# Performance work log

Measured on AMD Instinct MI355X. Metric: run time of the kernel, lower is better.

The kernel has to match this reference:

```python
import jax, jax.numpy as jnp
import numpy as np

# per-position segment id for seq_len=16: slices [0:1],[1:6],[6:9],[9:10],[10:16]
SEG = np.array([0] + [1]*5 + [2]*3 + [3] + [4]*6, dtype=np.int32)
HEAD_DIM = 3
NUM_HEADS = 2


def setup_inputs() -> dict:
    key = jax.random.key(0)
    ks = jax.random.split(key, 9)
    B = 262144
    s = 1.0 / np.sqrt(6.0)  # torch Linear init scale
    return {
        "x": jax.random.normal(ks[0], (B, 16, 6), dtype=jnp.float32),
        "Wq": jax.random.uniform(ks[1], (5, 6, 6), jnp.float32, -s, s),
        "bq": jax.random.uniform(ks[2], (5, 6), jnp.float32, -s, s),
        "Wk": jax.random.uniform(ks[3], (5, 6, 6), jnp.float32, -s, s),
        "bk": jax.random.uniform(ks[4], (5, 6), jnp.float32, -s, s),
        "Wv": jax.random.uniform(ks[5], (5, 6, 6), jnp.float32, -s, s),
        "bv": jax.random.uniform(ks[6], (5, 6), jnp.float32, -s, s),
        "Wo": jax.random.uniform(ks[7], (6, 6), jnp.float32, -s, s),
        "bo": jax.random.uniform(ks[8], (6,), jnp.float32, -s, s),
    }


def reference(x, Wq, bq, Wk, bk, Wv, bv, Wo, bo):
    B, S, D = x.shape  # S=16, D=6
    seg = jnp.asarray(SEG)

    def seg_proj(W, b):
        # torch Linear: y = x @ W.T + b; gather per-position segment weights
        return jnp.einsum('bsd,sod->bso', x, W[seg]) + b[seg]

    def heads(t):
        return t.reshape(B, S, NUM_HEADS, HEAD_DIM).transpose(0, 2, 1, 3)

    Q = heads(seg_proj(Wq, bq))  # [B,H,S,hd]
    K = heads(seg_proj(Wk, bk))
    V = heads(seg_proj(Wv, bv))

    scores = jnp.einsum('bhqd,bhkd->bhqk', Q, K) / jnp.sqrt(jnp.float32(HEAD_DIM))
    attn = jax.nn.softmax(scores, axis=-1)
    ctx = jnp.einsum('bhqk,bhkd->bhqd', attn, V)
    ctx = ctx.transpose(0, 2, 1, 3).reshape(B, S, D)
    return ctx @ Wo.T + bo
```

## Files before the change

### kernel.cpp

```cpp
#include <hip/hip_runtime.h>

#define SCALE 0.57735026918962576f

#define OFF_WQ 0
#define OFF_BQ 260
#define OFF_WK 300
#define OFF_BK 560
#define OFF_WV 600
#define OFF_BV 860
#define OFF_WO 900
#define OFF_BO 948
#define OFF_K  956
#define OFF_V  3068
#define GSTRIDE 132
#define LDS_FLOATS 5180

__global__ __launch_bounds__(256) void attn_seg_kernel(
    const float* __restrict__ x,
    const float* __restrict__ Wq, const float* __restrict__ bq,
    const float* __restrict__ Wk, const float* __restrict__ bk,
    const float* __restrict__ Wv, const float* __restrict__ bv,
    const float* __restrict__ Wo, const float* __restrict__ bo,
    float* __restrict__ out, int total)
{
    __shared__ __align__(16) float lds[LDS_FLOATS];
    const int t = threadIdx.x;

    if (t < 180) {
        unsigned sg = (unsigned)t / 36u, r = (unsigned)t - sg * 36u;
        unsigned o = r / 6u, d = r - o * 6u;
        int dst = (int)(sg * 52u + o * 8u + d);
        lds[OFF_WQ + dst] = Wq[t];
        lds[OFF_WK + dst] = Wk[t];
        lds[OFF_WV + dst] = Wv[t];
    }
    if (t < 30) {
        unsigned sg = (unsigned)t / 6u, o = (unsigned)t - sg * 6u;
        lds[OFF_BQ + sg * 8u + o] = bq[t];
        lds[OFF_BK + sg * 8u + o] = bk[t];
        lds[OFF_BV + sg * 8u + o] = bv[t];
    }
    if (t < 36) {
        unsigned o = (unsigned)t / 6u, d = (unsigned)t - o * 6u;
        lds[OFF_WO + o * 8u + d] = Wo[t];
    }
    if (t < 6) lds[OFF_BO + t] = bo[t];

    const int g = t >> 4;
    const int s = t & 15;
    const int seg = (s == 0) ? 0 : (s < 6) ? 1 : (s < 9) ? 2 : (s == 9) ? 3 : 4;

    const int pos = blockIdx.x * 256 + t;
    const bool valid = pos < total;
    float x0=0.f,x1=0.f,x2=0.f,x3=0.f,x4=0.f,x5=0.f;
    if (valid) {
        const float* xp = x + (size_t)pos * 6;
        float2 a = *(const float2*)(xp);
        float2 b = *(const float2*)(xp + 2);
        float2 c = *(const float2*)(xp + 4);
        x0=a.x; x1=a.y; x2=b.x; x3=b.y; x4=c.x; x5=c.y;
    }

    __syncthreads();

    float q[6], kk[6], vv[6];
    {
        const float* W = &lds[OFF_WQ + seg * 52];
        float4 b4 = *(const float4*)&lds[OFF_BQ + seg * 8];
        float2 b2 = *(const float2*)&lds[OFF_BQ + seg * 8 + 4];
        float bb[6] = {b4.x, b4.y, b4.z, b4.w, b2.x, b2.y};
        #pragma unroll
        for (int o = 0; o < 6; o++) {
            float4 w4 = *(const float4*)(W + o * 8);
            float2 w2 = *(const float2*)(W + o * 8 + 4);
            q[o] = bb[o] + x0*w4.x + x1*w4.y + x2*w4.z + x3*w4.w + x4*w2.x + x5*w2.y;
        }
    }
    {
        const float* W = &lds[OFF_WK + seg * 52];
        float4 b4 = *(const float4*)&lds[OFF_BK + seg * 8];
        float2 b2 = *(const float2*)&lds[OFF_BK + seg * 8 + 4];
        float bb[6] = {b4.x, b4.y, b4.z, b4.w, b2.x, b2.y};
        #pragma unroll
        for (int o = 0; o < 6; o++) {
            float4 w4 = *(const float4*)(W + o * 8);
            float2 w2 = *(const float2*)(W + o * 8 + 4);
            kk[o] = bb[o] + x0*w4.x + x1*w4.y + x2*w4.z + x3*w4.w + x4*w2.x + x5*w2.y;
        }
    }
    {
        const float* W = &lds[OFF_WV + seg * 52];
        float4 b4 = *(const float4*)&lds[OFF_BV + seg * 8];
        float2 b2 = *(const float2*)&lds[OFF_BV + seg * 8 + 4];
        float bb[6] = {b4.x, b4.y, b4.z, b4.w, b2.x, b2.y};
        #pragma unroll
        for (int o = 0; o < 6; o++) {
            float4 w4 = *(const float4*)(W + o * 8);
            float2 w2 = *(const float2*)(W + o * 8 + 4);
            vv[o] = bb[o] + x0*w4.x + x1*w4.y + x2*w4.z + x3*w4.w + x4*w2.x + x5*w2.y;
        }
    }

    {
        float* Kd = &lds[OFF_K + g * GSTRIDE + s * 8];
        *(float4*)Kd       = make_float4(kk[0], kk[1], kk[2], kk[3]);
        *(float2*)(Kd + 4) = make_float2(kk[4], kk[5]);
        float* Vd = &lds[OFF_V + g * GSTRIDE + s * 8];
        *(float4*)Vd       = make_float4(vv[0], vv[1], vv[2], vv[3]);
        *(float2*)(Vd + 4) = make_float2(vv[4], vv[5]);
    }

    __syncthreads();

    #pragma unroll
    for (int i = 0; i < 6; i++) q[i] *= SCALE;

    float sc0[16], sc1[16];
    {
        const float* Kb = &lds[OFF_K + g * GSTRIDE];
        #pragma unroll
        for (int k = 0; k < 16; k++) {
            float4 a = *(const float4*)(Kb + k * 8);
            float2 b = *(const float2*)(Kb + k * 8 + 4);
            sc0[k] = q[0]*a.x + q[1]*a.y + q[2]*a.z;
            sc1[k] = q[3]*a.w + q[4]*b.x + q[5]*b.y;
        }
    }

    float m0 = sc0[0], m1 = sc1[0];
    #pragma unroll
    for (int k = 1; k < 16; k++) { m0 = fmaxf(m0, sc0[k]); m1 = fmaxf(m1, sc1[k]); }
    float sum0 = 0.f, sum1 = 0.f;
    #pragma unroll
    for (int k = 0; k < 16; k++) {
        float e0 = __expf(sc0[k] - m0); sc0[k] = e0; sum0 += e0;
        float e1 = __expf(sc1[k] - m1); sc1[k] = e1; sum1 += e1;
    }
    const float inv0 = __builtin_amdgcn_rcpf(sum0);
    const float inv1 = __builtin_amdgcn_rcpf(sum1);

    float c0=0.f,c1=0.f,c2=0.f,c3=0.f,c4=0.f,c5=0.f;
    {
        const float* Vb = &lds[OFF_V + g * GSTRIDE];
        #pragma unroll
        for (int k = 0; k < 16; k++) {
            float4 a = *(const float4*)(Vb + k * 8);
            float2 b = *(const float2*)(Vb + k * 8 + 4);
            c0 += sc0[k]*a.x; c1 += sc0[k]*a.y; c2 += sc0[k]*a.z;
            c3 += sc1[k]*a.w; c4 += sc1[k]*b.x; c5 += sc1[k]*b.y;
        }
    }
    c0 *= inv0; c1 *= inv0; c2 *= inv0;
    c3 *= inv1; c4 *= inv1; c5 *= inv1;

    float4 bo4 = *(const float4*)&lds[OFF_BO];
    float2 bo2 = *(const float2*)&lds[OFF_BO + 4];
    float bos[6] = {bo4.x, bo4.y, bo4.z, bo4.w, bo2.x, bo2.y};
    float o_[6];
    #pragma unroll
    for (int o = 0; o < 6; o++) {
        float4 w4 = *(const float4*)&lds[OFF_WO + o * 8];
        float2 w2 = *(const float2*)&lds[OFF_WO + o * 8 + 4];
        o_[o] = bos[o] + c0*w4.x + c1*w4.y + c2*w4.z + c3*w4.w + c4*w2.x + c5*w2.y;
    }

    if (valid) {
        float* op = out + (size_t)pos * 6;
        *(float2*)(op)     = make_float2(o_[0], o_[1]);
        *(float2*)(op + 2) = make_float2(o_[2], o_[3]);
        *(float2*)(op + 4) = make_float2(o_[4], o_[5]);
    }
}

extern "C" void kernel_launch(void* const* d_in, const int* in_sizes, int n_in,
                              void* d_out, int out_size, void* d_ws, size_t ws_size,
                              hipStream_t stream) {
    const float* x  = (const float*)d_in[0];
    const float* Wq = (const float*)d_in[1];
    const float* bq = (const float*)d_in[2];
    const float* Wk = (const float*)d_in[3];
    const float* bk = (const float*)d_in[4];
    const float* Wv = (const float*)d_in[5];
    const float* bv = (const float*)d_in[6];
    const float* Wo = (const float*)d_in[7];
    const float* bo = (const float*)d_in[8];
    float* out = (float*)d_out;

    const int total = in_sizes[0] / 6;
    const int grid  = (total + 255) / 256;
    attn_seg_kernel<<<grid, 256, 0, stream>>>(x, Wq, bq, Wk, bk, Wv, bv, Wo, bo, out, total);
}
```

Before: 243.7 us.

## Process one batch element per thread with register-resident K/V and no LDS

Changes the mapping from one thread per sequence position to one thread per batch element. Each thread now computes all 16 K/V rows into registers and loops over queries, doing single-pass softmax with exp2 and a log2e-folded scale and no max subtraction. Weights are read directly from global/scalar memory instead of staged in LDS, and the barriers are removed. Per-thread global accesses become strided by 96 floats, which breaks coalescing. Register pressure is high, and dropping the max subtraction risks overflow on large scores.

```diff
diff --git a/kernel.cpp b/kernel.cpp
--- a/kernel.cpp
+++ b/kernel.cpp
@@ -1,174 +1,112 @@
 #include <hip/hip_runtime.h>
 
-#define SCALE 0.57735026918962576f
+#define QSCALE 0.83294038f
 
-#define OFF_WQ 0
-#define OFF_BQ 260
-#define OFF_WK 300
-#define OFF_BK 560
-#define OFF_WV 600
-#define OFF_BV 860
-#define OFF_WO 900
-#define OFF_BO 948
-#define OFF_K  956
-#define OFF_V  3068
-#define GSTRIDE 132
-#define LDS_FLOATS 5180
-
-__global__ __launch_bounds__(256) void attn_seg_kernel(
+__global__ __launch_bounds__(256, 2) void attn_seg_kernel(
     const float* __restrict__ x,
     const float* __restrict__ Wq, const float* __restrict__ bq,
     const float* __restrict__ Wk, const float* __restrict__ bk,
     const float* __restrict__ Wv, const float* __restrict__ bv,
     const float* __restrict__ Wo, const float* __restrict__ bo,
-    float* __restrict__ out, int total)
+    float* __restrict__ out, int nb)
 {
-    __shared__ __align__(16) float lds[LDS_FLOATS];
-    const int t = threadIdx.x;
+    const int b = blockIdx.x * 256 + threadIdx.x;
+    if (b >= nb) return;
 
-    if (t < 180) {
-        unsigned sg = (unsigned)t / 36u, r = (unsigned)t - sg * 36u;
-        unsigned o = r / 6u, d = r - o * 6u;
-        int dst = (int)(sg * 52u + o * 8u + d);
-        lds[OFF_WQ + dst] = Wq[t];
-        lds[OFF_WK + dst] = Wk[t];
-        lds[OFF_WV + dst] = Wv[t];
-    }
-    if (t < 30) {
-        unsigned sg = (unsigned)t / 6u, o = (unsigned)t - sg * 6u;
-        lds[OFF_BQ + sg * 8u + o] = bq[t];
-        lds[OFF_BK + sg * 8u + o] = bk[t];
-        lds[OFF_BV + sg * 8u + o] = bv[t];
-    }
-    if (t < 36) {
-        unsigned o = (unsigned)t / 6u, d = (unsigned)t - o * 6u;
-        lds[OFF_WO + o * 8u + d] = Wo[t];
-    }
-    if (t < 6) lds[OFF_BO + t] = bo[t];
+    const float* __restrict__ xb = x + (size_t)b * 96;
+    float* __restrict__ ob = out + (size_t)b * 96;
 
-    const int g = t >> 4;
-    const int s = t & 15;
-    const int seg = (s == 0) ? 0 : (s < 6) ? 1 : (s < 9) ? 2 : (s == 9) ? 3 : 4;
+    float K[16][6], V[16][6];
 
-    const int pos = blockIdx.x * 256 + t;
-    const bool valid = pos < total;
-    float x0=0.f,x1=0.f,x2=0.f,x3=0.f,x4=0.f,x5=0.f;
-    if (valid) {
-        const float* xp = x + (size_t)pos * 6;
-        float2 a = *(const float2*)(xp);
-        float2 b = *(const float2*)(xp + 2);
-        float2 c = *(const float2*)(xp + 4);
-        x0=a.x; x1=a.y; x2=b.x; x3=b.y; x4=c.x; x5=c.y;
-    }
-
-    __syncthreads();
-
-    float q[6], kk[6], vv[6];
-    {
-        const float* W = &lds[OFF_WQ + seg * 52];
-        float4 b4 = *(const float4*)&lds[OFF_BQ + seg * 8];
-        float2 b2 = *(const float2*)&lds[OFF_BQ + seg * 8 + 4];
-        float bb[6] = {b4.x, b4.y, b4.z, b4.w, b2.x, b2.y};
+    #pragma unroll
+    for (int sp = 0; sp < 8; ++sp) {
+        float4 A  = *(const float4*)(xb + sp * 12);
+        float4 Bq4 = *(const float4*)(xb + sp * 12 + 4);
+        float4 C  = *(const float4*)(xb + sp * 12 + 8);
+        float xr[2][6] = {{A.x, A.y, A.z, A.w, Bq4.x, Bq4.y},
+                          {Bq4.z, Bq4.w, C.x, C.y, C.z, C.w}};
         #pragma unroll
-        for (int o = 0; o < 6; o++) {
-            float4 w4 = *(const float4*)(W + o * 8);
-            float2 w2 = *(const float2*)(W + o * 8 + 4);
-            q[o] = bb[o] + x0*w4.x + x1*w4.y + x2*w4.z + x3*w4.w + x4*w2.x + x5*w2.y;
-        }
-    }
-    {
-        const float* W = &lds[OFF_WK + seg * 52];
-        float4 b4 = *(const float4*)&lds[OFF_BK + seg * 8];
-        float2 b2 = *(const float2*)&lds[OFF_BK + seg * 8 + 4];
-        float bb[6] = {b4.x, b4.y, b4.z, b4.w, b2.x, b2.y};
-        #pragma unroll
-        for (int o = 0; o < 6; o++) {
-            float4 w4 = *(const float4*)(W + o * 8);
-            float2 w2 = *(const float2*)(W + o * 8 + 4);
-            kk[o] = bb[o] + x0*w4.x + x1*w4.y + x2*w4.z + x3*w4.w + x4*w2.x + x5*w2.y;
-        }
-    }
-    {
-        const float* W = &lds[OFF_WV + seg * 52];
-        float4 b4 = *(const float4*)&lds[OFF_BV + seg * 8];
-        float2 b2 = *(const float2*)&lds[OFF_BV + seg * 8 + 4];
-        float bb[6] = {b4.x, b4.y, b4.z, b4.w, b2.x, b2.y};
-        #pragma unroll
-        for (int o = 0; o < 6; o++) {
-            float4 w4 = *(const float4*)(W + o * 8);
-            float2 w2 = *(const float2*)(W + o * 8 + 4);
-            vv[o] = bb[o] + x0*w4.x + x1*w4.y + x2*w4.z + x3*w4.w + x4*w2.x + x5*w2.y;
+        for (int h = 0; h < 2; ++h) {
+            const int s = sp * 2 + h;
+            const int sg = (s == 0) ? 0 : (s < 6) ? 1 : (s < 9) ? 2 : (s == 9) ? 3 : 4;
+            const float* wk = Wk + sg * 36;
+            const float* wv = Wv + sg * 36;
+            #pragma unroll
+            for (int j = 0; j < 6; ++j) {
+                float accK = bk[sg * 6 + j];
+                float accV = bv[sg * 6 + j];
+                #pragma unroll
+                for (int d = 0; d < 6; ++d) {
+                    accK += xr[h][d] * wk[j * 6 + d];
+                    accV += xr[h][d] * wv[j * 6 + d];
+                }
+                K[s][j] = accK;
+                V[s][j] = accV;
+            }
         }
     }
 
+    const float* xq = xb;
+    asm volatile("" : "+v"(xq));
+
+    float cx0, cx1, cx2, cx3, cx4, cx5;
     {
-        float* Kd = &lds[OFF_K + g * GSTRIDE + s * 8];
-        *(float4*)Kd       = make_float4(kk[0], kk[1], kk[2], kk[3]);
-        *(float2*)(Kd + 4) = make_float2(kk[4], kk[5]);
-        float* Vd = &lds[OFF_V + g * GSTRIDE + s * 8];
-        *(float4*)Vd       = make_float4(vv[0], vv[1], vv[2], vv[3]);
-        *(float2*)(Vd + 4) = make_float2(vv[4], vv[5]);
+        float2 a = *(const float2*)(xq);
+        float2 c = *(const float2*)(xq + 2);
+        float2 d = *(const float2*)(xq + 4);
+        cx0 = a.x; cx1 = a.y; cx2 = c.x; cx3 = c.y; cx4 = d.x; cx5 = d.y;
     }
 
-    __syncthreads();
+    #pragma unroll 1
+    for (int q = 0; q < 16; ++q) {
+        const float* pn = xq + ((q + 1) & 15) * 6;
+        float2 na = *(const float2*)(pn);
+        float2 nc = *(const float2*)(pn + 2);
+        float2 nd = *(const float2*)(pn + 4);
 
-    #pragma unroll
-    for (int i = 0; i < 6; i++) q[i] *= SCALE;
+        const int sg = (q == 0) ? 0 : (q < 6) ? 1 : (q < 9) ? 2 : (q == 9) ? 3 : 4;
+        const float* wq = Wq + sg * 36;
+        float qv[6];
+        #pragma unroll
+        for (int j = 0; j < 6; ++j) {
+            float acc = bq[sg * 6 + j];
+            acc += cx0 * wq[j * 6 + 0];
+            acc += cx1 * wq[j * 6 + 1];
+            acc += cx2 * wq[j * 6 + 2];
+            acc += cx3 * wq[j * 6 + 3];
+            acc += cx4 * wq[j * 6 + 4];
+            acc += cx5 * wq[j * 6 + 5];
+            qv[j] = acc * QSCALE;
+        }
 
-    float sc0[16], sc1[16];
-    {
-        const float* Kb = &lds[OFF_K + g * GSTRIDE];
+        float s0 = 0.f, s1 = 0.f;
+        float c0 = 0.f, c1 = 0.f, c2 = 0.f, c3 = 0.f, c4 = 0.f, c5 = 0.f;
         #pragma unroll
-        for (int k = 0; k < 16; k++) {
-            float4 a = *(const float4*)(Kb + k * 8);
-            float2 b = *(const float2*)(Kb + k * 8 + 4);
-            sc0[k] = q[0]*a.x + q[1]*a.y + q[2]*a.z;
-            sc1[k] = q[3]*a.w + q[4]*b.x + q[5]*b.y;
+        for (int k = 0; k < 16; ++k) {
+            float e0 = __builtin_amdgcn_exp2f(qv[0] * K[k][0] + qv[1] * K[k][1] + qv[2] * K[k][2]);
+            s0 += e0;
+            c0 += e0 * V[k][0]; c1 += e0 * V[k][1]; c2 += e0 * V[k][2];
+            float e1 = __builtin_amdgcn_exp2f(qv[3] * K[k][3] + qv[4] * K[k][4] + qv[5] * K[k][5]);
+            s1 += e1;
+            c3 += e1 * V[k][3]; c4 += e1 * V[k][4]; c5 += e1 * V[k][5];
         }
-    }
+        const float i0 = __builtin_amdgcn_rcpf(s0);
+        const float i1 = __builtin_amdgcn_rcpf(s1);
+        c0 *= i0; c1 *= i0; c2 *= i0;
+        c3 *= i1; c4 *= i1; c5 *= i1;
 
-    float m0 = sc0[0], m1 = sc1[0];
-    #pragma unroll
-    for (int k = 1; k < 16; k++) { m0 = fmaxf(m0, sc0[k]); m1 = fmaxf(m1, sc1[k]); }
-    float sum0 = 0.f, sum1 = 0.f;
-    #pragma unroll
-    for (int k = 0; k < 16; k++) {
-        float e0 = __expf(sc0[k] - m0); sc0[k] = e0; sum0 += e0;
-        float e1 = __expf(sc1[k] - m1); sc1[k] = e1; sum1 += e1;
-    }
-    const float inv0 = __builtin_amdgcn_rcpf(sum0);
-    const float inv1 = __builtin_amdgcn_rcpf(sum1);
-
-    float c0=0.f,c1=0.f,c2=0.f,c3=0.f,c4=0.f,c5=0.f;
-    {
-        const float* Vb = &lds[OFF_V + g * GSTRIDE];
+        float o_[6];
         #pragma unroll
-        for (int k = 0; k < 16; k++) {
-            float4 a = *(const float4*)(Vb + k * 8);
-            float2 b = *(const float2*)(Vb + k * 8 + 4);
-            c0 += sc0[k]*a.x; c1 += sc0[k]*a.y; c2 += sc0[k]*a.z;
-            c3 += sc1[k]*a.w; c4 += sc1[k]*b.x; c5 += sc1[k]*b.y;
+        for (int i = 0; i < 6; ++i) {
+            o_[i] = bo[i] + c0 * Wo[i * 6 + 0] + c1 * Wo[i * 6 + 1] + c2 * Wo[i * 6 + 2]
+                          + c3 * Wo[i * 6 + 3] + c4 * Wo[i * 6 + 4] + c5 * Wo[i * 6 + 5];
         }
-    }
-    c0 *= inv0; c1 *= inv0; c2 *= inv0;
-    c3 *= inv1; c4 *= inv1; c5 *= inv1;
-
-    float4 bo4 = *(const float4*)&lds[OFF_BO];
-    float2 bo2 = *(const float2*)&lds[OFF_BO + 4];
-    float bos[6] = {bo4.x, bo4.y, bo4.z, bo4.w, bo2.x, bo2.y};
-    float o_[6];
-    #pragma unroll
-    for (int o = 0; o < 6; o++) {
-        float4 w4 = *(const float4*)&lds[OFF_WO + o * 8];
-        float2 w2 = *(const float2*)&lds[OFF_WO + o * 8 + 4];
-        o_[o] = bos[o] + c0*w4.x + c1*w4.y + c2*w4.z + c3*w4.w + c4*w2.x + c5*w2.y;
-    }
-
-    if (valid) {
-        float* op = out + (size_t)pos * 6;
+        float* op = ob + q * 6;
         *(float2*)(op)     = make_float2(o_[0], o_[1]);
         *(float2*)(op + 2) = make_float2(o_[2], o_[3]);
         *(float2*)(op + 4) = make_float2(o_[4], o_[5]);
+
+        cx0 = na.x; cx1 = na.y; cx2 = nc.x; cx3 = nc.y; cx4 = nd.x; cx5 = nd.y;
     }
 }
 
@@ -186,7 +124,7 @@
     const float* bo = (const float*)d_in[8];
     float* out = (float*)d_out;
 
-    const int total = in_sizes[0] / 6;
-    const int grid  = (total + 255) / 256;
-    attn_seg_kernel<<<grid, 256, 0, stream>>>(x, Wq, bq, Wk, bk, Wv, bv, Wo, bo, out, total);
+    const int nb   = in_sizes[0] / 96;
+    const int grid = (nb + 255) / 256;
+    attn_seg_kernel<<<grid, 256, 0, stream>>>(x, Wq, bq, Wk, bk, Wv, bv, Wo, bo, out, nb);
 }
```

New measurement: 301.2 us. +23.6%, slower.
